# Optimization experiments

Measured on AMD Instinct MI355X. Metric: run time of the kernel, lower is better.

The kernel has to match this reference:

```python
import jax, jax.numpy as jnp
import numpy as np

N_GRAM = 4
D_STATE = 16
N_SLOTS = 500000
N_BLADES = 8
FNV_OFFSET = np.uint32(2166136261)
FNV_PRIME = np.uint32(16777619)


def setup_inputs() -> dict:
    key = jax.random.key(0)
    k1, k2 = jax.random.split(key)
    token_window = jax.random.randint(k1, (8, 8192, N_GRAM), 0, 50257, dtype=jnp.int32).astype(jnp.int64)
    bank = jax.random.normal(k2, (N_BLADES, N_SLOTS, D_STATE), dtype=jnp.float32)
    return {"token_window": token_window, "bank": bank}


def _fnv_address(token_window, n_slots):
    # FNV-1a over the n-gram window; uint32 wraparound == torch's % 2**32.
    tw = token_window.astype(jnp.uint32)
    h = jnp.full(tw.shape[:-1], FNV_OFFSET, dtype=jnp.uint32)
    for i in range(tw.shape[-1]):  # small fixed n_gram loop
        h = (h ^ tw[..., i]) * FNV_PRIME
    return (h % jnp.uint32(n_slots)).astype(jnp.int32)  # (B, S)


def reference(token_window, bank):
    # read_all_blades: hash-addressed gather across all 8 blade banks.
    addr = _fnv_address(token_window, bank.shape[1])  # (B, S)
    gathered = bank[:, addr, :]  # (8, B, S, d_state)
    return jnp.moveaxis(gathered, 0, -2)  # (B, S, 8, d_state)
```

## Files before the change

### kernel.cpp

```cpp
#include <hip/hip_runtime.h>
#include <stdint.h>

#define N_GRAM   4
#define D_STATE  16
#define N_SLOTS  500000
#define N_BLADES 8
#define N_POS    (8 * 8192)
#define FNV_OFFSET 2166136261u
#define FNV_PRIME  16777619u

__global__ __launch_bounds__(256) void TokenBladeBank_kernel(
    const int4* __restrict__ tok4,
    const float4* __restrict__ bank4,
    float4* __restrict__ out4)
{
    const int tid = blockIdx.x * blockDim.x + threadIdx.x;
    const int pos = tid >> 5;
    const int sub = tid & 31;
    if (pos >= N_POS) return;

    const int4 t = tok4[pos];

    uint32_t h = FNV_OFFSET;
    h = (h ^ (uint32_t)t.x) * FNV_PRIME;
    h = (h ^ (uint32_t)t.y) * FNV_PRIME;
    h = (h ^ (uint32_t)t.z) * FNV_PRIME;
    h = (h ^ (uint32_t)t.w) * FNV_PRIME;
    const uint32_t addr = h % (uint32_t)N_SLOTS;

    const int blade = sub >> 2;
    const int d4    = sub & 3;

    const float4 v = bank4[(size_t)blade * ((size_t)N_SLOTS * 4) + (size_t)addr * 4 + d4];

    out4[(size_t)pos * 32 + sub] = v;
}

extern "C" void kernel_launch(void* const* d_in, const int* in_sizes, int n_in,
                              void* d_out, int out_size, void* d_ws, size_t ws_size,
                              hipStream_t stream) {
    const int4*   tok4  = (const int4*)d_in[0];
    const float4* bank4 = (const float4*)d_in[1];
    float4*       out4  = (float4*)d_out;

    const int total_threads = N_POS * 32;
    const int block = 256;
    const int grid = (total_threads + block - 1) / block;

    TokenBladeBank_kernel<<<grid, block, 0, stream>>>(tok4, bank4, out4);
}
```

Before: 312.0 us.

## Relayout bank to slot-major in workspace before gathering contiguous rows

Adds a transpose kernel that uses LDS to rewrite the bank from blade-major to slot-major layout in the workspace, running on every call. A second kernel then gathers all eight blades for a hashed slot as one contiguous 512-byte row and writes the output with nontemporal stores. The aim is to replace eight scattered 64-byte reads per position with one contiguous read. The cost is a full read and write of the 256MB bank on each call, which may far outweigh the savings in the gather. If the workspace is missing or too small, the original direct kernel runs instead.

```diff
diff --git a/kernel.cpp b/kernel.cpp
--- a/kernel.cpp
+++ b/kernel.cpp
@@ -1,5 +1,6 @@
 #include <hip/hip_runtime.h>
 #include <stdint.h>
+#include <stddef.h>
 
 #define N_GRAM   4
 #define D_STATE  16
@@ -9,43 +10,115 @@
 #define FNV_OFFSET 2166136261u
 #define FNV_PRIME  16777619u
 
-__global__ __launch_bounds__(256) void TokenBladeBank_kernel(
-    const int4* __restrict__ tok4,
-    const float4* __restrict__ bank4,
-    float4* __restrict__ out4)
+typedef float v4f __attribute__((ext_vector_type(4)));
+typedef int   v4i __attribute__((ext_vector_type(4)));
+
+#define TSLOTS 64
+
+__global__ __launch_bounds__(256) void relayout_kernel(
+    const v4f* __restrict__ bank4,
+    v4f* __restrict__ ws4)
+{
+    __shared__ v4f lds[TSLOTS * 32];
+    const int t  = threadIdx.x;
+    const int s0 = blockIdx.x * TSLOTS;
+
+    #pragma unroll
+    for (int i = 0; i < 8; ++i) {
+        const int idx   = i * 256 + t;
+        const int blade = idx >> 8;
+        const int rem   = idx & 255;
+        const int slot  = rem >> 2;
+        const int d4    = rem & 3;
+        const int gs    = s0 + slot;
+        v4f v = {0.f, 0.f, 0.f, 0.f};
+        if (gs < N_SLOTS)
+            v = __builtin_nontemporal_load(
+                    &bank4[(size_t)blade * (N_SLOTS * 4) + (size_t)gs * 4 + d4]);
+        const int f = blade * 4 + d4;
+        lds[slot * 32 + (f ^ ((slot & 7) << 2))] = v;
+    }
+    __syncthreads();
+
+    #pragma unroll
+    for (int i = 0; i < 8; ++i) {
+        const int idx  = i * 256 + t;
+        const int slot = idx >> 5;
+        const int f    = idx & 31;
+        const int gs   = s0 + slot;
+        if (gs < N_SLOTS)
+            ws4[(size_t)gs * 32 + f] = lds[slot * 32 + (f ^ ((slot & 7) << 2))];
+    }
+}
+
+__global__ __launch_bounds__(256) void gather_kernel(
+    const v4i* __restrict__ tok4,
+    const v4f* __restrict__ ws4,
+    v4f* __restrict__ out4)
 {
     const int tid = blockIdx.x * blockDim.x + threadIdx.x;
     const int pos = tid >> 5;
     const int sub = tid & 31;
     if (pos >= N_POS) return;
 
-    const int4 t = tok4[pos];
+    const v4i tk = tok4[pos];
 
     uint32_t h = FNV_OFFSET;
-    h = (h ^ (uint32_t)t.x) * FNV_PRIME;
-    h = (h ^ (uint32_t)t.y) * FNV_PRIME;
-    h = (h ^ (uint32_t)t.z) * FNV_PRIME;
-    h = (h ^ (uint32_t)t.w) * FNV_PRIME;
+    h = (h ^ (uint32_t)tk.x) * FNV_PRIME;
+    h = (h ^ (uint32_t)tk.y) * FNV_PRIME;
+    h = (h ^ (uint32_t)tk.z) * FNV_PRIME;
+    h = (h ^ (uint32_t)tk.w) * FNV_PRIME;
+    const uint32_t addr = h % (uint32_t)N_SLOTS;
+
+    const v4f v = ws4[(size_t)addr * 32 + sub];
+    __builtin_nontemporal_store(v, &out4[(size_t)pos * 32 + sub]);
+}
+
+__global__ __launch_bounds__(256) void direct_kernel(
+    const v4i* __restrict__ tok4,
+    const v4f* __restrict__ bank4,
+    v4f* __restrict__ out4)
+{
+    const int tid = blockIdx.x * blockDim.x + threadIdx.x;
+    const int pos = tid >> 5;
+    const int sub = tid & 31;
+    if (pos >= N_POS) return;
+
+    const v4i tk = tok4[pos];
+
+    uint32_t h = FNV_OFFSET;
+    h = (h ^ (uint32_t)tk.x) * FNV_PRIME;
+    h = (h ^ (uint32_t)tk.y) * FNV_PRIME;
+    h = (h ^ (uint32_t)tk.z) * FNV_PRIME;
+    h = (h ^ (uint32_t)tk.w) * FNV_PRIME;
     const uint32_t addr = h % (uint32_t)N_SLOTS;
 
     const int blade = sub >> 2;
     const int d4    = sub & 3;
-
-    const float4 v = bank4[(size_t)blade * ((size_t)N_SLOTS * 4) + (size_t)addr * 4 + d4];
-
+    const v4f v = bank4[(size_t)blade * ((size_t)N_SLOTS * 4) + (size_t)addr * 4 + d4];
     out4[(size_t)pos * 32 + sub] = v;
 }
 
 extern "C" void kernel_launch(void* const* d_in, const int* in_sizes, int n_in,
                               void* d_out, int out_size, void* d_ws, size_t ws_size,
                               hipStream_t stream) {
-    const int4*   tok4  = (const int4*)d_in[0];
-    const float4* bank4 = (const float4*)d_in[1];
-    float4*       out4  = (float4*)d_out;
+    const v4i* tok4  = (const v4i*)d_in[0];
+    const v4f* bank4 = (const v4f*)d_in[1];
+    v4f*       out4  = (v4f*)d_out;
 
-    const int total_threads = N_POS * 32;
-    const int block = 256;
-    const int grid = (total_threads + block - 1) / block;
+    const size_t need = (size_t)N_SLOTS * N_BLADES * D_STATE * sizeof(float);
 
-    TokenBladeBank_kernel<<<grid, block, 0, stream>>>(tok4, bank4, out4);
+    if (d_ws != nullptr && ws_size >= need) {
+        v4f* ws4 = (v4f*)d_ws;
+        const int grid1 = (N_SLOTS + TSLOTS - 1) / TSLOTS;
+        relayout_kernel<<<grid1, 256, 0, stream>>>(bank4, ws4);
+
+        const int total_threads = N_POS * 32;
+        const int grid2 = (total_threads + 255) / 256;
+        gather_kernel<<<grid2, 256, 0, stream>>>(tok4, ws4, out4);
+    } else {
+        const int total_threads = N_POS * 32;
+        const int grid = (total_threads + 255) / 256;
+        direct_kernel<<<grid, 256, 0, stream>>>(tok4, bank4, out4);
+    }
 }
```

New measurement: 391.8 us. 1.26x slower.
